# Kernel tuning notes

Hardware: AMD Instinct MI355X
Metric: run time of the kernel (lower is better)

## Reference

```python
import jax, jax.numpy as jnp
import numpy as np
import math

D_EMBED, D_K, N_HEADS = 1024, 1024, 16
D_H = D_EMBED // N_HEADS          # 64
ROT_DIM = D_H // 2                # 32, RotaryEmbedding(dim=d_h//2)
B, LQ, LK = 2, 2048, 2048


def _rope_freqs(seq_len):
    # lucidrains rotary-embedding-torch: inv_freq over half of `dim`, interleave-repeated
    inv_freq = 1.0 / (10000.0 ** (jnp.arange(0, ROT_DIM, 2, dtype=jnp.float32) / ROT_DIM))
    t = jnp.arange(seq_len, dtype=jnp.float32)
    f = t[:, None] * inv_freq[None, :]          # [S, ROT_DIM/2]
    return jnp.repeat(f, 2, axis=-1)            # [S, ROT_DIM] interleaved


def _apply_rotary(x, freqs):
    # x: [B,H,S,D_H]; rotate first ROT_DIM features, pass the rest through
    x_rot, x_pass = x[..., :ROT_DIM], x[..., ROT_DIM:]
    cos, sin = jnp.cos(freqs), jnp.sin(freqs)   # [S, ROT_DIM]
    x1, x2 = x_rot[..., 0::2], x_rot[..., 1::2]
    rotated = jnp.stack((-x2, x1), axis=-1).reshape(x_rot.shape)
    return jnp.concatenate([x_rot * cos + rotated * sin, x_pass], axis=-1)


def setup_inputs() -> dict:
    key = jax.random.key(0)
    ks = jax.random.split(key, 12)
    s = 0.02
    return {
        "embed": jax.random.normal(ks[0], (B, LQ, D_EMBED), jnp.float32),
        "key": jax.random.normal(ks[1], (B, LK, D_K), jnp.float32),
        "attn_mask": jnp.ones((B, LQ, LK), dtype=bool),
        "WQ": jax.random.normal(ks[2], (D_EMBED, D_EMBED), jnp.float32) * s,
        "bQ": jnp.zeros((D_EMBED,), jnp.float32),
        "WK": jax.random.normal(ks[3], (D_K, D_EMBED), jnp.float32) * s,
        "bK": jnp.zeros((D_EMBED,), jnp.float32),
        "WV": jax.random.normal(ks[4], (D_K, D_EMBED), jnp.float32) * s,
        "bV": jnp.zeros((D_EMBED,), jnp.float32),
        "WO": jax.random.normal(ks[5], (D_EMBED, D_EMBED), jnp.float32) * s,
        "bO": jnp.zeros((D_EMBED,), jnp.float32),
    }


def reference(embed, key, attn_mask, WQ, bQ, WK, bK, WV, bV, WO, bO):
    bsz, len_q, _ = embed.shape
    len_k = key.shape[1]
    scale = 1.0 / math.sqrt(D_EMBED)  # note: module scales by 1/sqrt(d_embed)

    Q = embed @ WQ + bQ
    K = key @ WK + bK
    V = key @ WV + bV

    # [B, H, S, D_H]
    Qh = Q.reshape(bsz, len_q, N_HEADS, D_H).transpose(0, 2, 1, 3)
    Kh = K.reshape(bsz, len_k, N_HEADS, D_H).transpose(0, 2, 1, 3)
    Vh = V.reshape(bsz, len_k, N_HEADS, D_H).transpose(0, 2, 1, 3)

    Qh = _apply_rotary(Qh, _rope_freqs(len_q))
    Kh = _apply_rotary(Kh, _rope_freqs(len_k))

    attn = jnp.einsum('bhqd,bhkd->bhqk', Qh, Kh)
    attn = jnp.where(attn_mask[:, None, :, :], attn, -jnp.inf)
    attn = jax.nn.softmax(attn * scale, axis=-1)

    out = jnp.einsum('bhqk,bhkd->bhqd', attn, Vh)
    out = out.transpose(0, 2, 1, 3).reshape(bsz, len_q, D_EMBED)
    return out @ WO + bO
```

## Files before the change

### kernel.cpp

```cpp
#include <hip/hip_runtime.h>
#include <hip/hip_bf16.h>
#include <cstdint>
#include <cstddef>

typedef __bf16 bf16_t;
typedef bf16_t bf16x8 __attribute__((ext_vector_type(8)));
typedef bf16_t bf16x4 __attribute__((ext_vector_type(4)));
typedef bf16_t bf16x2 __attribute__((ext_vector_type(2)));
typedef float f32x4 __attribute__((ext_vector_type(4)));
typedef float f32x16 __attribute__((ext_vector_type(16)));
typedef unsigned int u32x4 __attribute__((ext_vector_type(4)));

namespace {
constexpr int Bv = 2, Lv = 2048, Ev = 1024, NHv = 16;
constexpr int Mv = Bv * Lv;
constexpr float SCALE_L2E = 0.03125f * 1.4426950408889634f;
}

__device__ __forceinline__ void gload_lds16(const void* g, void* l) {
  __builtin_amdgcn_global_load_lds(
      (const __attribute__((address_space(1))) unsigned int*)g,
      (__attribute__((address_space(3))) unsigned int*)l,
      16, 0, 0);
}

__global__ __launch_bounds__(256) void k_cvt2(const float* __restrict__ x0,
                                              const float* __restrict__ x1,
                                              bf16_t* __restrict__ y0,
                                              bf16_t* __restrict__ y1, int n4) {
  const float* x = blockIdx.z ? x1 : x0;
  bf16_t* y = blockIdx.z ? y1 : y0;
  int i = blockIdx.x * 256 + threadIdx.x;
  if (i < n4) {
    float4 v = reinterpret_cast<const float4*>(x)[i];
    bf16x4 o = {(bf16_t)v.x, (bf16_t)v.y, (bf16_t)v.z, (bf16_t)v.w};
    *reinterpret_cast<bf16x4*>(&y[(size_t)i * 4]) = o;
  }
}

__global__ __launch_bounds__(256) void k_twt(const float* w0, const float* w1,
                                             const float* w2, const float* w3,
                                             bf16_t* t0, bf16_t* t1,
                                             bf16_t* t2, bf16_t* t3) {
  const float* W;
  bf16_t* T;
  switch (blockIdx.z) {
    case 0: W = w0; T = t0; break;
    case 1: W = w1; T = t1; break;
    case 2: W = w2; T = t2; break;
    default: W = w3; T = t3; break;
  }
  __shared__ float tile[32][33];
  const int tx = threadIdx.x, ty = threadIdx.y;
  const int n0 = blockIdx.x * 32, k0 = blockIdx.y * 32;
#pragma unroll
  for (int i = 0; i < 4; i++) {
    int r = ty + i * 8;
    tile[r][tx] = W[(size_t)(k0 + r) * Ev + n0 + tx];
  }
  __syncthreads();
#pragma unroll
  for (int i = 0; i < 4; i++) {
    int r = ty + i * 8;
    T[(size_t)(n0 + r) * Ev + k0 + tx] = (bf16_t)tile[tx][r];
  }
}

__global__ __launch_bounds__(256) void k_trig(float2* __restrict__ tab) {
  int t = blockIdx.x * 256 + threadIdx.x;
  int i = t & 15, l = t >> 4;
  float inv = exp2f(-13.287712379549449f * (float)i * (1.0f / 16.0f));
  float s, c;
  sincosf((float)l * inv, &s, &c);
  tab[t] = make_float2(c, s);
}

__global__ __launch_bounds__(256) void k_gemm_qkv(
    const bf16_t* __restrict__ Ae, const bf16_t* __restrict__ Ak,
    const bf16_t* __restrict__ WtQ, const bf16_t* __restrict__ WtK,
    const bf16_t* __restrict__ WtV, const float* __restrict__ bQ,
    const float* __restrict__ bK, const float* __restrict__ bV,
    const float2* __restrict__ tab, bf16_t* __restrict__ Qbf,
    bf16_t* __restrict__ Kbf, bf16_t* __restrict__ Vtr) {
  constexpr int K = Ev;
  const int z = blockIdx.z;
  const bf16_t* A = (z == 0) ? Ae : Ak;
  const bf16_t* Bt = (z == 0) ? WtQ : (z == 1) ? WtK : WtV;
  const float* bias = (z == 0) ? bQ : (z == 1) ? bK : bV;

  __shared__ __align__(16) bf16_t As[128 * 32];
  __shared__ __align__(16) bf16_t Bs[128 * 32];
  const int tid = threadIdx.x;
  const int wid = tid >> 6, lane = tid & 63;
  const int bm = blockIdx.y * 128, bn = blockIdx.x * 128;
  const int wr = wid >> 1, wc = wid & 1;
  f32x4 acc[4][4] = {};
  const int srow = wid * 32 + (lane >> 2);
  const int scol = (lane & 3) * 8;
  const size_t ga0 = (size_t)(bm + srow) * K + scol;
  const size_t ga1 = (size_t)(bm + srow + 16) * K + scol;
  const size_t gb0 = (size_t)(bn + srow) * K + scol;
  const size_t gb1 = (size_t)(bn + srow + 16) * K + scol;
  bf16_t* asw = &As[wid * 1024];
  bf16_t* bsw = &Bs[wid * 1024];
  for (int k0 = 0; k0 < K; k0 += 32) {
    gload_lds16(A + ga0 + k0, asw);
    gload_lds16(A + ga1 + k0, asw + 512);
    gload_lds16(Bt + gb0 + k0, bsw);
    gload_lds16(Bt + gb1 + k0, bsw + 512);
    __syncthreads();
    bf16x8 af[4], bfr[4];
#pragma unroll
    for (int m = 0; m < 4; m++)
      af[m] = *(const bf16x8*)&As[(wr * 64 + m * 16 + (lane & 15)) * 32 + (lane >> 4) * 8];
#pragma unroll
    for (int n = 0; n < 4; n++)
      bfr[n] = *(const bf16x8*)&Bs[(wc * 64 + n * 16 + (lane & 15)) * 32 + (lane >> 4) * 8];
#pragma unroll
    for (int m = 0; m < 4; m++)
#pragma unroll
      for (int n = 0; n < 4; n++)
        acc[m][n] = __builtin_amdgcn_mfma_f32_16x16x32_bf16(af[m], bfr[n], acc[m][n], 0, 0, 0);
    __syncthreads();
  }

  const int l15 = lane & 15, g = lane >> 4;
  if (z == 2) {
#pragma unroll
    for (int n = 0; n < 4; n++) {
      const int col = bn + wc * 64 + n * 16 + l15;
      const int hh = (col >> 6) & 15;
      const int d = col & 63;
      const float bv = bias[col];
#pragma unroll
      for (int m = 0; m < 4; m++) {
        const int row0 = bm + wr * 64 + m * 16 + (g << 2);
        const int b = row0 >> 11, l0 = row0 & 2047;
        bf16x4 ov;
#pragma unroll
        for (int r = 0; r < 4; r++) ov[r] = (bf16_t)(acc[m][n][r] + bv);
        *(bf16x4*)&Vtr[((size_t)((b * NHv + hh) * 64 + d)) * Lv + l0] = ov;
      }
    }
    return;
  }

  bf16_t* Y = (z == 0) ? Qbf : Kbf;
  const float scale = (z == 0) ? SCALE_L2E : 1.0f;
  const float ssign = (l15 & 1) ? 1.0f : -1.0f;
#pragma unroll
  for (int n = 0; n < 4; n++) {
    const int col = bn + wc * 64 + n * 16 + l15;
    const int h = (col >> 6) & 15;
    const int d = col & 63;
    const float bv = bias[col];
    const bool dorope = (d < 32);
    const int ti = d >> 1;
#pragma unroll
    for (int m = 0; m < 4; m++) {
      const int row0 = bm + wr * 64 + m * 16 + (g << 2);
#pragma unroll
      for (int r = 0; r < 4; r++) {
        const int row = row0 + r;
        const int l = row & 2047, b = row >> 11;
        float v = acc[m][n][r] + bv;
        float p = __shfl_xor(v, 1);
        float o = v;
        if (dorope) {
          float2 cs = tab[(l << 4) + ti];
          o = v * cs.x + p * cs.y * ssign;
        }
        Y[(((size_t)(b * NHv + h)) * Lv + l) * 64 + d] = (bf16_t)(o * scale);
      }
    }
  }
}

__global__ __launch_bounds__(256) void k_gemm_bt(const bf16_t* __restrict__ A,
                                                 const bf16_t* __restrict__ Bt,
                                                 const float* __restrict__ bias,
                                                 float* __restrict__ C,
                                                 int N, int K) {
  __shared__ __align__(16) bf16_t As[128 * 32];
  __shared__ __align__(16) bf16_t Bs[128 * 32];
  const int tid = threadIdx.x;
  const int wid = tid >> 6, lane = tid & 63;
  const int bm = blockIdx.y * 128, bn = blockIdx.x * 128;
  const int wr = wid >> 1, wc = wid & 1;
  f32x4 acc[4][4] = {};
  const int srow = wid * 32 + (lane >> 2);
  const int scol = (lane & 3) * 8;
  const size_t ga0 = (size_t)(bm + srow) * K + scol;
  const size_t ga1 = (size_t)(bm + srow + 16) * K + scol;
  const size_t gb0 = (size_t)(bn + srow) * K + scol;
  const size_t gb1 = (size_t)(bn + srow + 16) * K + scol;
  bf16_t* asw = &As[wid * 1024];
  bf16_t* bsw = &Bs[wid * 1024];
  for (int k0 = 0; k0 < K; k0 += 32) {
    gload_lds16(A + ga0 + k0, asw);
    gload_lds16(A + ga1 + k0, asw + 512);
    gload_lds16(Bt + gb0 + k0, bsw);
    gload_lds16(Bt + gb1 + k0, bsw + 512);
    __syncthreads();
    bf16x8 af[4], bfr[4];
#pragma unroll
    for (int m = 0; m < 4; m++)
      af[m] = *(const bf16x8*)&As[(wr * 64 + m * 16 + (lane & 15)) * 32 + (lane >> 4) * 8];
#pragma unroll
    for (int n = 0; n < 4; n++)
      bfr[n] = *(const bf16x8*)&Bs[(wc * 64 + n * 16 + (lane & 15)) * 32 + (lane >> 4) * 8];
#pragma unroll
    for (int m = 0; m < 4; m++)
#pragma unroll
      for (int n = 0; n < 4; n++)
        acc[m][n] = __builtin_amdgcn_mfma_f32_16x16x32_bf16(af[m], bfr[n], acc[m][n], 0, 0, 0);
    __syncthreads();
  }
#pragma unroll
  for (int n = 0; n < 4; n++) {
    const int col = bn + wc * 64 + n * 16 + (lane & 15);
    const float bv = bias[col];
#pragma unroll
    for (int m = 0; m < 4; m++) {
      const int row0 = bm + wr * 64 + m * 16 + ((lane >> 4) << 2);
#pragma unroll
      for (int r = 0; r < 4; r++)
        C[(size_t)(row0 + r) * N + col] = acc[m][n][r] + bv;
    }
  }
}

__global__ void k_flag_init(int* f) { f[0] = 1; f[1] = 1; }

__global__ __launch_bounds__(256) void k_mask_and(const unsigned int* __restrict__ m,
                                                  int* __restrict__ f, int nwords) {
  int i = blockIdx.x * 256 + threadIdx.x;
  const int u8words = nwords >> 2;
  bool badA = false, badB = false;
  for (; i < nwords; i += gridDim.x * 256) {
    unsigned int v = m[i];
    badA |= (i < u8words) & (v != 0x01010101u);
    badB |= (v != 1u);
  }
  if (__any(badA) && (threadIdx.x & 63) == 0) f[0] = 0;
  if (__any(badB) && (threadIdx.x & 63) == 0) f[1] = 0;
}

__device__ __forceinline__ void flash_stage(const bf16_t* __restrict__ Kg,
                                            const bf16_t* __restrict__ Vg,
                                            bf16_t* ksb, bf16_t* vsb,
                                            int tid, int kt) {
#pragma unroll
  for (int i = 0; i < 2; i++) {
    int slot = i * 256 + tid;
    int r = slot >> 3, c = slot & 7;
    int sb = ((c * 16) ^ ((r & 7) << 4)) >> 1;
    bf16_t* dk = ksb + (size_t)(i * 256 + (tid & 192)) * 8;
    gload_lds16(Kg + (size_t)(kt * 64 + r) * 64 + sb, dk);
    bf16_t* dv = vsb + (size_t)(i * 256 + (tid & 192)) * 8;
    gload_lds16(Vg + (size_t)r * Lv + kt * 64 + sb, dv);
  }
}

__global__ __launch_bounds__(256) void k_flash32(const bf16_t* __restrict__ Qh,
                                                 const bf16_t* __restrict__ Kh,
                                                 const bf16_t* __restrict__ Vtr,
                                                 const int* __restrict__ mask,
                                                 const int* __restrict__ allflag,
                                                 bf16_t* __restrict__ Oh) {
  __shared__ __align__(16) bf16_t Ks[2][64 * 64];
  __shared__ __align__(16) bf16_t Vs[2][64 * 64];
  __shared__ float sw[4][32];
  const int tid = threadIdx.x, wid = tid >> 6, lane = tid & 63;
  const int l31 = lane & 31, hf = lane >> 5;
  const int qt = blockIdx.x, bh = blockIdx.y;
  const int b = bh >> 4, hd = bh & 15;
  const size_t base = (size_t)bh * Lv * 64;
  const bf16_t* Kg = Kh + base;
  const bf16_t* Vg = Vtr + base;
  const int allm = allflag[0] | allflag[1];
  const int q = qt * 128 + wid * 32 + l31;

  bf16x8 bq[4];
#pragma unroll
  for (int s = 0; s < 4; s++)
    bq[s] = *(const bf16x8*)&Qh[base + (size_t)q * 64 + s * 16 + hf * 8];

  float m_r = -INFINITY, l_p = 0.f;
  f32x16 o0 = {}, o1 = {};
  const int xsw = (l31 & 7) << 4;

  flash_stage(Kg, Vg, Ks[0], Vs[0], tid, 0);
  __syncthreads();
  int cur = 0;
  for (int kt = 0; kt < Lv / 64; ++kt) {
    if (kt + 1 < Lv / 64)
      flash_stage(Kg, Vg, Ks[cur ^ 1], Vs[cur ^ 1], tid, kt + 1);
    const bf16_t* KsC = Ks[cur];
    const bf16_t* VsC = Vs[cur];

    f32x16 st0 = {}, st1 = {};
    __builtin_amdgcn_s_setprio(1);
#pragma unroll
    for (int s = 0; s < 4; s++) {
      const int eo = (((s * 16 + hf * 8) * 2) ^ xsw) >> 1;
      bf16x8 k0 = *(const bf16x8*)&KsC[l31 * 64 + eo];
      bf16x8 k1 = *(const bf16x8*)&KsC[(32 + l31) * 64 + eo];
      st0 = __builtin_amdgcn_mfma_f32_32x32x16_bf16(k0, bq[s], st0, 0, 0, 0);
      st1 = __builtin_amdgcn_mfma_f32_32x32x16_bf16(k1, bq[s], st1, 0, 0, 0);
    }
    __builtin_amdgcn_s_setprio(0);

    if (!allm) {
      const int* mrow = &mask[(size_t)b * Lv * Lv + (size_t)q * Lv + kt * 64];
#pragma unroll
      for (int r = 0; r < 16; r++) {
        const int kv = (r & 3) + 8 * (r >> 2) + 4 * hf;
        if (!mrow[kv]) st0[r] = -INFINITY;
        if (!mrow[32 + kv]) st1[r] = -INFINITY;
      }
    }

    float pm = st0[0];
#pragma unroll
    for (int r = 1; r < 16; r++) pm = fmaxf(pm, st0[r]);
#pragma unroll
    for (int r = 0; r < 16; r++) pm = fmaxf(pm, st1[r]);
    if (__any(pm > m_r + 8.0f)) {
      float pmf = fmaxf(pm, __shfl_xor(pm, 32));
      float mn = fmaxf(m_r, pmf);
      float alpha = exp2f(m_r - mn);
      m_r = mn;
      l_p *= alpha;
      if (!hf) sw[wid][l31] = alpha;
      asm volatile("s_waitcnt lgkmcnt(0)" ::: "memory");
      __builtin_amdgcn_sched_barrier(0);
#pragma unroll
      for (int r = 0; r < 16; r++) {
        float a = sw[wid][(r & 3) + 8 * (r >> 2) + 4 * hf];
        o0[r] *= a;
        o1[r] *= a;
      }
    }
    float ps = 0.f;
#pragma unroll
    for (int r = 0; r < 16; r++) {
      float p = exp2f(st0[r] - m_r);
      st0[r] = p;
      ps += p;
    }
#pragma unroll
    for (int r = 0; r < 16; r++) {
      float p = exp2f(st1[r] - m_r);
      st1[r] = p;
      ps += p;
    }
    l_p += ps;

    unsigned int pk0[8], pk1[8];
#pragma unroll
    for (int i = 0; i < 8; i++) {
      float a0 = st0[2 * i], a1 = st0[2 * i + 1];
      float b0 = st1[2 * i], b1 = st1[2 * i + 1];
      asm("v_cvt_pk_bf16_f32 %0, %1, %2" : "=v"(pk0[i]) : "v"(a0), "v"(a1));
      asm("v_cvt_pk_bf16_f32 %0, %1, %2" : "=v"(pk1[i]) : "v"(b0), "v"(b1));
    }

    __builtin_amdgcn_s_setprio(1);
#pragma unroll
    for (int s = 0; s < 4; s++) {
      const int c = 4 * (s & 1);
      unsigned int w0, w1, w2, w3;
      if (s >> 1) {
        w0 = pk1[c + 0]; w1 = pk1[c + 1]; w2 = pk1[c + 2]; w3 = pk1[c + 3];
      } else {
        w0 = pk0[c + 0]; w1 = pk0[c + 1]; w2 = pk0[c + 2]; w3 = pk0[c + 3];
      }
      unsigned int sel0 = hf ? w0 : w2;
      unsigned int sel1 = hf ? w1 : w3;
      unsigned int x0 = (unsigned int)__shfl_xor((int)sel0, 32);
      unsigned int x1 = (unsigned int)__shfl_xor((int)sel1, 32);
      u32x4 u;
      u[0] = hf ? x0 : w0;
      u[1] = hf ? x1 : w1;
      u[2] = hf ? w2 : x0;
      u[3] = hf ? w3 : x1;
      bf16x8 pa = __builtin_bit_cast(bf16x8, u);
      const int eo = (((s * 16 + hf * 8) * 2) ^ xsw) >> 1;
      bf16x8 v0 = *(const bf16x8*)&VsC[l31 * 64 + eo];
      bf16x8 v1 = *(const bf16x8*)&VsC[(32 + l31) * 64 + eo];
      o0 = __builtin_amdgcn_mfma_f32_32x32x16_bf16(pa, v0, o0, 0, 0, 0);
      o1 = __builtin_amdgcn_mfma_f32_32x32x16_bf16(pa, v1, o1, 0, 0, 0);
    }
    __builtin_amdgcn_s_setprio(0);

    __syncthreads();
    cur ^= 1;
  }

  float lt = l_p + __shfl_xor(l_p, 32);
  if (!hf) sw[wid][l31] = 1.0f / lt;
  asm volatile("s_waitcnt lgkmcnt(0)" ::: "memory");
  __builtin_amdgcn_sched_barrier(0);
#pragma unroll
  for (int r = 0; r < 16; r++) {
    const int rq = (r & 3) + 8 * (r >> 2) + 4 * hf;
    float inv = sw[wid][rq];
    const int qg = qt * 128 + wid * 32 + rq;
    const size_t off = ((size_t)(b * Lv + qg)) * Ev + hd * 64;
    Oh[off + l31] = (bf16_t)(o0[r] * inv);
    Oh[off + 32 + l31] = (bf16_t)(o1[r] * inv);
  }
}

extern "C" void kernel_launch(void* const* d_in, const int* in_sizes, int n_in,
                              void* d_out, int out_size, void* d_ws, size_t ws_size,
                              hipStream_t stream) {
  const float* embed = (const float*)d_in[0];
  const float* key = (const float*)d_in[1];
  const int* mask = (const int*)d_in[2];
  const float* WQ = (const float*)d_in[3];
  const float* bQ = (const float*)d_in[4];
  const float* WK = (const float*)d_in[5];
  const float* bK = (const float*)d_in[6];
  const float* WV = (const float*)d_in[7];
  const float* bV = (const float*)d_in[8];
  const float* WO = (const float*)d_in[9];
  const float* bO = (const float*)d_in[10];
  float* out = (float*)d_out;
  char* ws = (char*)d_ws;
  const size_t MB = 1024 * 1024;

  bf16_t* Wt = (bf16_t*)(ws);
  bf16_t* Ae = (bf16_t*)(ws + 8 * MB);
  bf16_t* Ak = (bf16_t*)(ws + 16 * MB);
  bf16_t* Qbf = (bf16_t*)(ws + 40 * MB);
  bf16_t* Kbf = (bf16_t*)(ws + 48 * MB);
  bf16_t* Vtr = (bf16_t*)(ws + 56 * MB);
  bf16_t* AO = (bf16_t*)(ws + 8 * MB);
  int* flag = (int*)(ws + 64 * MB);
  float2* tab = (float2*)(ws + 65 * MB);

  {
    dim3 cg(4096, 1, 2);
    k_cvt2<<<cg, 256, 0, stream>>>(embed, key, Ae, Ak, Mv * Ev / 4);
  }
  {
    dim3 tb(32, 8), tg(32, 32, 4);
    k_twt<<<tg, tb, 0, stream>>>(WQ, WK, WV, WO, Wt, Wt + 1024 * 1024,
                                 Wt + 2 * 1024 * 1024, Wt + 3 * 1024 * 1024);
  }
  k_trig<<<128, 256, 0, stream>>>(tab);
  k_flag_init<<<1, 1, 0, stream>>>(flag);
  k_mask_and<<<2048, 256, 0, stream>>>((const unsigned int*)mask, flag,
                                       Bv * Lv * Lv);

  {
    dim3 gg(8, 32, 3);
    k_gemm_qkv<<<gg, 256, 0, stream>>>(Ae, Ak, Wt, Wt + 1024 * 1024,
                                       Wt + 2 * 1024 * 1024, bQ, bK, bV, tab,
                                       Qbf, Kbf, Vtr);
  }
  {
    dim3 fg(16, 32);
    k_flash32<<<fg, 256, 0, stream>>>(Qbf, Kbf, Vtr, mask, flag, AO);
  }
  {
    dim3 gg(8, 32);
    k_gemm_bt<<<gg, 256, 0, stream>>>(AO, Wt + 3 * 1024 * 1024, bO, out, Ev, Ev);
  }
}
```

Measured before the change: 188.4 us.

## Load K/V tiles directly from global into registers in flash kernel

Removes the shared-memory double-buffered K/V staging (global_load_lds plus swizzled LDS reads and per-tile barriers) and has each wave read its K and V fragments straight from global memory into registers every tile. This removes the LDS traffic and the __syncthreads between tiles. In exchange, the four waves of a block now each fetch the same K/V data separately, relying on L1/L2 to absorb the reuse, and nothing prefetches the next tile, so global latency is only hidden by occupancy. Register pressure also grows from the 16 bf16x8 fragments held per iteration.

```diff
diff --git a/kernel.cpp b/kernel.cpp
--- a/kernel.cpp
+++ b/kernel.cpp
@@ -246,38 +246,18 @@
   if (__any(badB) && (threadIdx.x & 63) == 0) f[1] = 0;
 }
 
-__device__ __forceinline__ void flash_stage(const bf16_t* __restrict__ Kg,
-                                            const bf16_t* __restrict__ Vg,
-                                            bf16_t* ksb, bf16_t* vsb,
-                                            int tid, int kt) {
-#pragma unroll
-  for (int i = 0; i < 2; i++) {
-    int slot = i * 256 + tid;
-    int r = slot >> 3, c = slot & 7;
-    int sb = ((c * 16) ^ ((r & 7) << 4)) >> 1;
-    bf16_t* dk = ksb + (size_t)(i * 256 + (tid & 192)) * 8;
-    gload_lds16(Kg + (size_t)(kt * 64 + r) * 64 + sb, dk);
-    bf16_t* dv = vsb + (size_t)(i * 256 + (tid & 192)) * 8;
-    gload_lds16(Vg + (size_t)r * Lv + kt * 64 + sb, dv);
-  }
-}
-
 __global__ __launch_bounds__(256) void k_flash32(const bf16_t* __restrict__ Qh,
                                                  const bf16_t* __restrict__ Kh,
                                                  const bf16_t* __restrict__ Vtr,
                                                  const int* __restrict__ mask,
                                                  const int* __restrict__ allflag,
                                                  bf16_t* __restrict__ Oh) {
-  __shared__ __align__(16) bf16_t Ks[2][64 * 64];
-  __shared__ __align__(16) bf16_t Vs[2][64 * 64];
   __shared__ float sw[4][32];
   const int tid = threadIdx.x, wid = tid >> 6, lane = tid & 63;
   const int l31 = lane & 31, hf = lane >> 5;
   const int qt = blockIdx.x, bh = blockIdx.y;
   const int b = bh >> 4, hd = bh & 15;
   const size_t base = (size_t)bh * Lv * 64;
-  const bf16_t* Kg = Kh + base;
-  const bf16_t* Vg = Vtr + base;
   const int allm = allflag[0] | allflag[1];
   const int q = qt * 128 + wid * 32 + l31;
 
@@ -286,28 +266,30 @@
   for (int s = 0; s < 4; s++)
     bq[s] = *(const bf16x8*)&Qh[base + (size_t)q * 64 + s * 16 + hf * 8];
 
+  const bf16_t* kp = Kh + base + (size_t)l31 * 64 + hf * 8;
+  const bf16_t* vp = Vtr + base + (size_t)l31 * Lv + hf * 8;
+
   float m_r = -INFINITY, l_p = 0.f;
   f32x16 o0 = {}, o1 = {};
-  const int xsw = (l31 & 7) << 4;
-
-  flash_stage(Kg, Vg, Ks[0], Vs[0], tid, 0);
-  __syncthreads();
-  int cur = 0;
+
   for (int kt = 0; kt < Lv / 64; ++kt) {
-    if (kt + 1 < Lv / 64)
-      flash_stage(Kg, Vg, Ks[cur ^ 1], Vs[cur ^ 1], tid, kt + 1);
-    const bf16_t* KsC = Ks[cur];
-    const bf16_t* VsC = Vs[cur];
+    bf16x8 k0[4], k1[4], v0[4], v1[4];
+    const bf16_t* kt0 = kp + (size_t)kt * 4096;
+    const bf16_t* vt0 = vp + kt * 64;
+#pragma unroll
+    for (int s = 0; s < 4; s++) {
+      k0[s] = *(const bf16x8*)(kt0 + s * 16);
+      k1[s] = *(const bf16x8*)(kt0 + 2048 + s * 16);
+      v0[s] = *(const bf16x8*)(vt0 + s * 16);
+      v1[s] = *(const bf16x8*)(vt0 + (size_t)32 * Lv + s * 16);
+    }
 
     f32x16 st0 = {}, st1 = {};
     __builtin_amdgcn_s_setprio(1);
 #pragma unroll
     for (int s = 0; s < 4; s++) {
-      const int eo = (((s * 16 + hf * 8) * 2) ^ xsw) >> 1;
-      bf16x8 k0 = *(const bf16x8*)&KsC[l31 * 64 + eo];
-      bf16x8 k1 = *(const bf16x8*)&KsC[(32 + l31) * 64 + eo];
-      st0 = __builtin_amdgcn_mfma_f32_32x32x16_bf16(k0, bq[s], st0, 0, 0, 0);
-      st1 = __builtin_amdgcn_mfma_f32_32x32x16_bf16(k1, bq[s], st1, 0, 0, 0);
+      st0 = __builtin_amdgcn_mfma_f32_32x32x16_bf16(k0[s], bq[s], st0, 0, 0, 0);
+      st1 = __builtin_amdgcn_mfma_f32_32x32x16_bf16(k1[s], bq[s], st1, 0, 0, 0);
     }
     __builtin_amdgcn_s_setprio(0);
 
@@ -386,16 +368,10 @@
       u[2] = hf ? w2 : x0;
       u[3] = hf ? w3 : x1;
       bf16x8 pa = __builtin_bit_cast(bf16x8, u);
-      const int eo = (((s * 16 + hf * 8) * 2) ^ xsw) >> 1;
-      bf16x8 v0 = *(const bf16x8*)&VsC[l31 * 64 + eo];
-      bf16x8 v1 = *(const bf16x8*)&VsC[(32 + l31) * 64 + eo];
-      o0 = __builtin_amdgcn_mfma_f32_32x32x16_bf16(pa, v0, o0, 0, 0, 0);
-      o1 = __builtin_amdgcn_mfma_f32_32x32x16_bf16(pa, v1, o1, 0, 0, 0);
+      o0 = __builtin_amdgcn_mfma_f32_32x32x16_bf16(pa, v0[s], o0, 0, 0, 0);
+      o1 = __builtin_amdgcn_mfma_f32_32x32x16_bf16(pa, v1[s], o1, 0, 0, 0);
     }
     __builtin_amdgcn_s_setprio(0);
-
-    __syncthreads();
-    cur ^= 1;
   }
 
   float lt = l_p + __shfl_xor(l_p, 32);
```

After: 232.4 us. +23.4%, slower.

## Permute V-transpose key order to drop cross-half shuffles in PV MFMA

Applied to the files above, without the earlier changes.

The V projection epilogue now writes V-transposed with a permuted key order within each 16-key group, swapping the two middle 4-key chunks. Because V's layout now matches the register layout of the packed P accumulators, the flash kernel feeds pk0/pk1 straight into the PV MFMA and drops the per-step __shfl_xor exchanges and selects. The swizzled LDS offsets are also computed once outside the loop. This couples the projection layout to the attention consumer, and correctness depends on the permutation exactly matching the MFMA output row mapping.

```diff
diff --git a/kernel.cpp b/kernel.cpp
--- a/kernel.cpp
+++ b/kernel.cpp
@@ -136,10 +136,13 @@
       for (int m = 0; m < 4; m++) {
         const int row0 = bm + wr * 64 + m * 16 + (g << 2);
         const int b = row0 >> 11, l0 = row0 & 2047;
+        const int pq = (l0 >> 2) & 3;
+        const int pq2 = ((pq & 1) << 1) | (pq >> 1);
+        const int l0p = (l0 & ~12) | (pq2 << 2);
         bf16x4 ov;
 #pragma unroll
         for (int r = 0; r < 4; r++) ov[r] = (bf16_t)(acc[m][n][r] + bv);
-        *(bf16x4*)&Vtr[((size_t)((b * NHv + hh) * 64 + d)) * Lv + l0] = ov;
+        *(bf16x4*)&Vtr[((size_t)((b * NHv + hh) * 64 + d)) * Lv + l0p] = ov;
       }
     }
     return;
@@ -286,9 +289,13 @@
   for (int s = 0; s < 4; s++)
     bq[s] = *(const bf16x8*)&Qh[base + (size_t)q * 64 + s * 16 + hf * 8];
 
+  const int xsw = (l31 & 7) << 4;
+  int eo_[4];
+#pragma unroll
+  for (int s = 0; s < 4; s++) eo_[s] = (((s * 16 + hf * 8) * 2) ^ xsw) >> 1;
+
   float m_r = -INFINITY, l_p = 0.f;
   f32x16 o0 = {}, o1 = {};
-  const int xsw = (l31 & 7) << 4;
 
   flash_stage(Kg, Vg, Ks[0], Vs[0], tid, 0);
   __syncthreads();
@@ -303,9 +310,8 @@
     __builtin_amdgcn_s_setprio(1);
 #pragma unroll
     for (int s = 0; s < 4; s++) {
-      const int eo = (((s * 16 + hf * 8) * 2) ^ xsw) >> 1;
-      bf16x8 k0 = *(const bf16x8*)&KsC[l31 * 64 + eo];
-      bf16x8 k1 = *(const bf16x8*)&KsC[(32 + l31) * 64 + eo];
+      bf16x8 k0 = *(const bf16x8*)&KsC[l31 * 64 + eo_[s]];
+      bf16x8 k1 = *(const bf16x8*)&KsC[(32 + l31) * 64 + eo_[s]];
       st0 = __builtin_amdgcn_mfma_f32_32x32x16_bf16(k0, bq[s], st0, 0, 0, 0);
       st1 = __builtin_amdgcn_mfma_f32_32x32x16_bf16(k1, bq[s], st1, 0, 0, 0);
     }
@@ -369,26 +375,19 @@
     __builtin_amdgcn_s_setprio(1);
 #pragma unroll
     for (int s = 0; s < 4; s++) {
-      const int c = 4 * (s & 1);
-      unsigned int w0, w1, w2, w3;
-      if (s >> 1) {
-        w0 = pk1[c + 0]; w1 = pk1[c + 1]; w2 = pk1[c + 2]; w3 = pk1[c + 3];
+      u32x4 u;
+      if (s == 0) {
+        u[0] = pk0[0]; u[1] = pk0[1]; u[2] = pk0[2]; u[3] = pk0[3];
+      } else if (s == 1) {
+        u[0] = pk0[4]; u[1] = pk0[5]; u[2] = pk0[6]; u[3] = pk0[7];
+      } else if (s == 2) {
+        u[0] = pk1[0]; u[1] = pk1[1]; u[2] = pk1[2]; u[3] = pk1[3];
       } else {
-        w0 = pk0[c + 0]; w1 = pk0[c + 1]; w2 = pk0[c + 2]; w3 = pk0[c + 3];
+        u[0] = pk1[4]; u[1] = pk1[5]; u[2] = pk1[6]; u[3] = pk1[7];
       }
-      unsigned int sel0 = hf ? w0 : w2;
-      unsigned int sel1 = hf ? w1 : w3;
-      unsigned int x0 = (unsigned int)__shfl_xor((int)sel0, 32);
-      unsigned int x1 = (unsigned int)__shfl_xor((int)sel1, 32);
-      u32x4 u;
-      u[0] = hf ? x0 : w0;
-      u[1] = hf ? x1 : w1;
-      u[2] = hf ? w2 : x0;
-      u[3] = hf ? w3 : x1;
       bf16x8 pa = __builtin_bit_cast(bf16x8, u);
-      const int eo = (((s * 16 + hf * 8) * 2) ^ xsw) >> 1;
-      bf16x8 v0 = *(const bf16x8*)&VsC[l31 * 64 + eo];
-      bf16x8 v1 = *(const bf16x8*)&VsC[(32 + l31) * 64 + eo];
+      bf16x8 v0 = *(const bf16x8*)&VsC[l31 * 64 + eo_[s]];
+      bf16x8 v1 = *(const bf16x8*)&VsC[(32 + l31) * 64 + eo_[s]];
       o0 = __builtin_amdgcn_mfma_f32_32x32x16_bf16(pa, v0, o0, 0, 0, 0);
       o1 = __builtin_amdgcn_mfma_f32_32x32x16_bf16(pa, v1, o1, 0, 0, 0);
     }
```

Measured after the change: 180.1 us. 1.05x faster.
